# Performance work log

Measured on AMD Instinct MI355X. Metric: run time of the kernel, lower is better.

Reference implementation:

```python
import jax, jax.numpy as jnp
import numpy as np

N = 50000        # nodes
E = 1600000      # edges (before self loops)
IN_DIM = 300     # input feature size
HID = 256        # hidden size
HEADS = 8
OC = HID // HEADS  # out channels per head = 32
LAYERS = 4
B = 1024         # number of target pairs
C = 3            # num classes
NEG_SLOPE = 0.2  # PyG GATConv leaky_relu slope


def setup_inputs() -> dict:
    key = jax.random.key(0)
    ks = jax.random.split(key, 12)

    def glorot(k, shape):
        lim = np.sqrt(6.0 / (shape[-2] + shape[-1]))
        return jax.random.uniform(k, shape, jnp.float32, -lim, lim)

    return {
        "x": jax.random.normal(ks[0], (N, IN_DIM), jnp.float32),
        "edge_index": jax.random.randint(ks[1], (2, E), 0, N, jnp.int64 if jax.config.jax_enable_x64 else jnp.int32),
        "target_mask": jax.random.randint(ks[2], (B, 2), 0, N, jnp.int64 if jax.config.jax_enable_x64 else jnp.int32),
        # lin1: [IN_DIM, HID] (stored pre-transposed vs torch)
        "lin1_W": glorot(ks[3], (IN_DIM, HID)),
        "lin1_b": jnp.zeros((HID,), jnp.float32),
        # stacked GATConv params
        "convs_W": glorot(ks[4], (LAYERS, HID, HEADS * OC)),
        "convs_att_dst": glorot(ks[5], (LAYERS, HEADS, OC)),  # att half applied to x_i (target)
        "convs_att_src": glorot(ks[6], (LAYERS, HEADS, OC)),  # att half applied to x_j (source)
        "convs_b": jnp.zeros((LAYERS, HID), jnp.float32),
        # lin3: [2*HID, C]
        "lin3_W": glorot(ks[7], (2 * HID, C)),
        "lin3_b": jnp.zeros((C,), jnp.float32),
    }


def gat_layer(h, src, tgt, W, att_dst, att_src, bias):
    """PyG-style GATConv (concat heads), edge list already includes self loops.
    h: [N, HID]; src/tgt: [E+N]; W: [HID, HEADS*OC]."""
    hw = (h @ W).reshape(N, HEADS, OC)
    # per-node attention scores, gathered per-edge (avoids materializing concat features)
    s_dst = jnp.einsum("nho,ho->nh", hw, att_dst)  # score for target role
    s_src = jnp.einsum("nho,ho->nh", hw, att_src)  # score for source role
    alpha = jax.nn.leaky_relu(s_dst[tgt] + s_src[src], NEG_SLOPE)  # [Etot, HEADS]
    # softmax over edges sharing the same target node (self loops => no empty segments)
    m = jax.ops.segment_max(alpha, tgt, num_segments=N)
    ex = jnp.exp(alpha - m[tgt])
    denom = jax.ops.segment_sum(ex, tgt, num_segments=N)
    a = ex / (denom[tgt] + 1e-16)
    # weighted scatter-aggregate of source features
    out = jax.ops.segment_sum(hw[src] * a[:, :, None], tgt, num_segments=N)  # [N, HEADS, OC]
    return out.reshape(N, HEADS * OC) + bias


def reference(x, edge_index, target_mask, lin1_W, lin1_b, convs_W,
              convs_att_dst, convs_att_src, convs_b, lin3_W, lin3_b):
    # add self loops once (PyG GATConv does this per layer; same edge set every layer)
    loop = jnp.arange(N, dtype=edge_index.dtype)
    src = jnp.concatenate([edge_index[0], loop])
    tgt = jnp.concatenate([edge_index[1], loop])

    h = x @ lin1_W + lin1_b
    for l in range(LAYERS):
        h = jax.nn.elu(gat_layer(h, src, tgt, convs_W[l],
                                 convs_att_dst[l], convs_att_src[l], convs_b[l]))
    # gather the two target nodes per sample and flatten -> [B, 2*HID]
    feats = h[target_mask].reshape(B, 2 * HID)
    logits = feats @ lin3_W + lin3_b
    return logits
```

## Files before the change

kernel.cpp:

```cpp
#include <hip/hip_runtime.h>
#include <math.h>

#define N_NODES 50000
#define N_PAD   50048
#define E_EDGES 1600000
#define ETOT    (E_EDGES + N_NODES)
#define EPAD    (E_EDGES + 8 * N_NODES)
#define IN_DIM  300
#define KP1     320
#define HID     256
#define HEADS   8
#define OC      32
#define LAYERS  4
#define BSAMP   1024
#define NEG_SLOPE 0.2f
#define DEG_CAP 128

typedef _Float16 half8 __attribute__((ext_vector_type(8)));
typedef _Float16 half4v __attribute__((ext_vector_type(4)));
typedef float f32x4 __attribute__((ext_vector_type(4)));


__global__ __launch_bounds__(256) void init_counts_kernel(int* counts) {
    int i = blockIdx.x * 256 + threadIdx.x;
    if (i < N_NODES) counts[i] = 1;
}

__global__ __launch_bounds__(256) void count_edges_kernel(const int* __restrict__ tgt, int* counts) {
    int e = blockIdx.x * 256 + threadIdx.x;
    if (e < E_EDGES) atomicAdd(&counts[tgt[e]], 1);
}

__global__ __launch_bounds__(256) void scan_kernel(const int* __restrict__ counts,
                                                   int* __restrict__ row_ptr,
                                                   int* __restrict__ cursor) {
    __shared__ int sums[256];
    const int CHUNK = (N_NODES + 255) / 256;
    int t = threadIdx.x;
    int beg = t * CHUNK;
    int fin = min(beg + CHUNK, N_NODES);
    int s = 0;
    for (int i = beg; i < fin; i++) s += (counts[i] + 7) & ~7;
    sums[t] = s;
    __syncthreads();
    for (int off = 1; off < 256; off <<= 1) {
        int a = sums[t];
        int u = (t >= off) ? sums[t - off] : 0;
        __syncthreads();
        sums[t] = a + u;
        __syncthreads();
    }
    int running = sums[t] - s;
    for (int i = beg; i < fin; i++) {
        row_ptr[i] = running;
        cursor[i]  = running;
        running += (counts[i] + 7) & ~7;
    }
    if (t == 255) row_ptr[N_NODES] = sums[255];
}

__global__ __launch_bounds__(256) void fill_edges_kernel(const int* __restrict__ src,
                                                         const int* __restrict__ tgt,
                                                         int* cursor, int* __restrict__ col) {
    int e = blockIdx.x * 256 + threadIdx.x;
    if (e >= ETOT) return;
    int s_, t_;
    if (e < E_EDGES) { s_ = src[e]; t_ = tgt[e]; }
    else             { s_ = t_ = e - E_EDGES; }
    int pos = atomicAdd(&cursor[t_], 1);
    col[pos] = s_;
}

__global__ __launch_bounds__(256) void pad_edges_kernel(const int* __restrict__ cursor,
                                                        const int* __restrict__ row_ptr,
                                                        int* __restrict__ col) {
    int i = blockIdx.x * 256 + threadIdx.x;
    if (i >= N_NODES) return;
    int e = cursor[i];
    int pe = row_ptr[i + 1];
    for (; e < pe; e++) col[e] = i;
}


__global__ __launch_bounds__(256) void cast_x_kernel(const float* __restrict__ x, _Float16* __restrict__ xh) {
    long i = (long)blockIdx.x * 256 + threadIdx.x;
    if (i >= (long)N_NODES * KP1) return;
    int r = (int)(i / KP1), c = (int)(i % KP1);
    float v = (c < IN_DIM) ? x[(size_t)r * IN_DIM + c] : 0.f;
    xh[i] = (_Float16)v;
}

__global__ __launch_bounds__(256) void cast_w1_kernel(const float* __restrict__ W, _Float16* __restrict__ Wt) {
    int i = blockIdx.x * 256 + threadIdx.x;
    if (i >= HID * KP1) return;
    int n = i / KP1, k = i % KP1;
    float v = (k < IN_DIM) ? W[(size_t)k * HID + n] : 0.f;
    Wt[i] = (_Float16)v;
}

__global__ __launch_bounds__(256) void cast_wc_kernel(const float* __restrict__ W, _Float16* __restrict__ Wt) {
    int i = blockIdx.x * 256 + threadIdx.x;
    if (i >= LAYERS * HID * HID) return;
    int l = i / (HID * HID);
    int r = i % (HID * HID);
    int n = r / HID, k = r % HID;
    Wt[i] = (_Float16)W[(size_t)l * HID * HID + (size_t)k * HID + n];
}

__global__ __launch_bounds__(256) void gemm_mfma_kernel(const _Float16* __restrict__ A,
                                                        const _Float16* __restrict__ Wt,
                                                        const float* __restrict__ bias,
                                                        _Float16* __restrict__ C,
                                                        int M, int Kp, int addbias) {
    __shared__ _Float16 As[128][32];
    __shared__ _Float16 Bs[128][32];
    const int tid = threadIdx.x;
    const int m0 = blockIdx.x * 128;
    const int n0 = blockIdx.y * 128;
    const int w = tid >> 6, lane = tid & 63;
    const int wm = (w & 1) * 64, wn = (w >> 1) * 64;
    const int quad = lane >> 4, m16 = lane & 15;

    f32x4 acc[4][4];
    #pragma unroll
    for (int i = 0; i < 4; i++)
        #pragma unroll
        for (int j = 0; j < 4; j++)
            acc[i][j] = (f32x4){0.f, 0.f, 0.f, 0.f};

    for (int k0 = 0; k0 < Kp; k0 += 32) {
        #pragma unroll
        for (int i = 0; i < 2; i++) {
            int seg = tid + i * 256;
            int row = seg >> 2, off = seg & 3;
            uint4 v = *(const uint4*)&A[(size_t)(m0 + row) * Kp + k0 + off * 8];
            *(uint4*)&As[row][off * 8] = v;
            uint4 u = *(const uint4*)&Wt[(size_t)(n0 + row) * Kp + k0 + off * 8];
            *(uint4*)&Bs[row][off * 8] = u;
        }
        __syncthreads();

        half8 af[4], bf[4];
        #pragma unroll
        for (int i = 0; i < 4; i++) {
            af[i] = *(const half8*)&As[wm + i * 16 + m16][quad * 8];
            bf[i] = *(const half8*)&Bs[wn + i * 16 + m16][quad * 8];
        }
        #pragma unroll
        for (int mi = 0; mi < 4; mi++)
            #pragma unroll
            for (int ni = 0; ni < 4; ni++)
                acc[mi][ni] = __builtin_amdgcn_mfma_f32_16x16x32_f16(af[mi], bf[ni], acc[mi][ni], 0, 0, 0);
        __syncthreads();
    }

    #pragma unroll
    for (int mi = 0; mi < 4; mi++) {
        #pragma unroll
        for (int r = 0; r < 4; r++) {
            int row = m0 + wm + mi * 16 + quad * 4 + r;
            if (row < M) {
                #pragma unroll
                for (int ni = 0; ni < 4; ni++) {
                    int colg = n0 + wn + ni * 16 + m16;
                    float v = acc[mi][ni][r];
                    if (addbias) v += bias[colg];
                    C[(size_t)row * HID + colg] = (_Float16)v;
                }
            }
        }
    }
}

__global__ __launch_bounds__(256) void score_kernel(const _Float16* __restrict__ hw,
                                                    const float* __restrict__ att_dst,
                                                    const float* __restrict__ att_src,
                                                    float* __restrict__ s_dst,
                                                    float* __restrict__ s_src) {
    int n = blockIdx.x;
    int c = threadIdx.x;
    float v  = (float)hw[(size_t)n * HID + c];
    float vd = v * att_dst[c];
    float vs = v * att_src[c];
    #pragma unroll
    for (int off = 16; off >= 1; off >>= 1) {
        vd += __shfl_xor(vd, off);
        vs += __shfl_xor(vs, off);
    }
    if ((c & 31) == 0) {
        int h = c >> 5;
        s_dst[(size_t)n * HEADS + h] = vd;
        s_src[(size_t)n * HEADS + h] = vs;
    }
}

__global__ __launch_bounds__(256) void agg_kernel(const int* __restrict__ row_ptr,
                                                  const int* __restrict__ deg_arr,
                                                  const int* __restrict__ col,
                                                  const float* __restrict__ s_dst,
                                                  const float* __restrict__ s_src,
                                                  const _Float16* __restrict__ hw,
                                                  const float* __restrict__ bias,
                                                  _Float16* __restrict__ h_out) {
    __shared__ float aL[4][DEG_CAP * 8];
    __shared__ int  snL[4][DEG_CAP];

    int wv   = threadIdx.x >> 6;
    int lane = threadIdx.x & 63;
    int t = blockIdx.x * 4 + wv;
    if (t >= N_NODES) return;

    int start = row_ptr[t];
    int pdeg  = row_ptr[t + 1] - start;
    int deg   = deg_arr[t];

    int eh  = lane & 7;
    int ech = lane >> 3;
    float sd = s_dst[(size_t)t * HEADS + eh];

    if (pdeg <= DEG_CAP) {
        float mx = -1e30f;
        int ngrp = pdeg >> 3;
        for (int g = 0; g < ngrp; g++) {
            int slot = g * 8 + ech;
            int sn = col[start + slot];
            float a = sd + s_src[(size_t)sn * HEADS + eh];
            a = (a > 0.f) ? a : NEG_SLOPE * a;
            aL[wv][slot * 8 + eh] = a;
            if (eh == 0) snL[wv][slot] = sn;
            if (slot < deg) mx = fmaxf(mx, a);
        }
        mx = fmaxf(mx, __shfl_xor(mx, 8));
        mx = fmaxf(mx, __shfl_xor(mx, 16));
        mx = fmaxf(mx, __shfl_xor(mx, 32));

        int p  = lane >> 5;
        int c  = lane & 31;
        int hh = c >> 2;
        float mxc = __shfl(mx, hh);

        const half8* hw8 = (const half8*)hw;
        float acc[8] = {0.f, 0.f, 0.f, 0.f, 0.f, 0.f, 0.f, 0.f};
        float dsum = 0.f;

        for (int g = 0; g < ngrp; g++) {
            int base = g * 8;
            int   sns[4];
            half8 v[4];
            float ex[4];
            #pragma unroll
            for (int j = 0; j < 4; j++) sns[j] = snL[wv][base + 2 * j + p];
            #pragma unroll
            for (int j = 0; j < 4; j++) v[j] = hw8[(size_t)sns[j] * 32 + c];
            #pragma unroll
            for (int j = 0; j < 4; j++) {
                int slot = base + 2 * j + p;
                float a = aL[wv][slot * 8 + hh];
                ex[j] = (slot < deg) ? __expf(a - mxc) : 0.f;
                dsum += ex[j];
            }
            #pragma unroll
            for (int j = 0; j < 4; j++)
                #pragma unroll
                for (int i = 0; i < 8; i++)
                    acc[i] += ex[j] * (float)v[j][i];
        }

        dsum += __shfl_xor(dsum, 32);
        #pragma unroll
        for (int i = 0; i < 8; i++) acc[i] += __shfl_xor(acc[i], 32);

        float inv = 1.f / (dsum + 1e-16f);
        if (p == 0) {
            half8 ov;
            #pragma unroll
            for (int i = 0; i < 8; i++) {
                float o = acc[i] * inv + bias[c * 8 + i];
                o = (o > 0.f) ? o : (__expf(o) - 1.f);
                ov[i] = (_Float16)o;
            }
            ((half8*)h_out)[(size_t)t * 32 + c] = ov;
        }
    } else {
        int end = start + deg;
        float mx = -1e30f;
        for (int base = start; base < end; base += 8) {
            int e = base + ech;
            if (e < end) {
                int sn = col[e];
                float a = sd + s_src[(size_t)sn * HEADS + eh];
                a = (a > 0.f) ? a : NEG_SLOPE * a;
                mx = fmaxf(mx, a);
            }
        }
        mx = fmaxf(mx, __shfl_xor(mx, 8));
        mx = fmaxf(mx, __shfl_xor(mx, 16));
        mx = fmaxf(mx, __shfl_xor(mx, 32));

        float4 acc = {0.f, 0.f, 0.f, 0.f};
        float dsum = 0.f;
        const half4v* hw4 = (const half4v*)hw;
        int chead = lane >> 3;
        for (int base = start; base < end; base += 8) {
            int e = base + ech;
            float exv = 0.f;
            int sn = 0;
            if (e < end) {
                sn = col[e];
                float a = sd + s_src[(size_t)sn * HEADS + eh];
                a = (a > 0.f) ? a : NEG_SLOPE * a;
                exv = __expf(a - mx);
                dsum += exv;
            }
            int cnt = min(8, end - base);
            for (int j = 0; j < cnt; j++) {
                float exj = __shfl(exv, j * 8 + chead);
                int  snj  = __shfl(sn,  j * 8);
                half4v v = hw4[(size_t)snj * 64 + lane];
                acc.x += exj * (float)v[0];
                acc.y += exj * (float)v[1];
                acc.z += exj * (float)v[2];
                acc.w += exj * (float)v[3];
            }
        }
        dsum += __shfl_xor(dsum, 8);
        dsum += __shfl_xor(dsum, 16);
        dsum += __shfl_xor(dsum, 32);
        float den = __shfl(dsum, chead) + 1e-16f;
        float inv = 1.f / den;
        int cb = lane * 4;
        float o[4] = {acc.x * inv + bias[cb + 0], acc.y * inv + bias[cb + 1],
                      acc.z * inv + bias[cb + 2], acc.w * inv + bias[cb + 3]};
        #pragma unroll
        for (int i = 0; i < 4; i++) o[i] = (o[i] > 0.f) ? o[i] : (__expf(o[i]) - 1.f);
        half4v ov;
        ov[0] = (_Float16)o[0]; ov[1] = (_Float16)o[1];
        ov[2] = (_Float16)o[2]; ov[3] = (_Float16)o[3];
        ((half4v*)h_out)[(size_t)t * 64 + lane] = ov;
    }
}

__global__ __launch_bounds__(256) void head_kernel(const _Float16* __restrict__ h,
                                                   const int* __restrict__ target_mask,
                                                   const float* __restrict__ W,
                                                   const float* __restrict__ b,
                                                   float* __restrict__ out) {
    int s = blockIdx.x;
    int t = threadIdx.x;
    int n0 = target_mask[s * 2 + 0];
    int n1 = target_mask[s * 2 + 1];
    float f0 = (float)h[(size_t)n0 * HID + t];
    float f1 = (float)h[(size_t)n1 * HID + t];
    float a0 = f0 * W[t * 3 + 0] + f1 * W[(t + 256) * 3 + 0];
    float a1 = f0 * W[t * 3 + 1] + f1 * W[(t + 256) * 3 + 1];
    float a2 = f0 * W[t * 3 + 2] + f1 * W[(t + 256) * 3 + 2];
    #pragma unroll
    for (int off = 32; off >= 1; off >>= 1) {
        a0 += __shfl_xor(a0, off);
        a1 += __shfl_xor(a1, off);
        a2 += __shfl_xor(a2, off);
    }
    __shared__ float red[4][3];
    int wv = t >> 6, ln = t & 63;
    if (ln == 0) { red[wv][0] = a0; red[wv][1] = a1; red[wv][2] = a2; }
    __syncthreads();
    if (t < 3) {
        out[s * 3 + t] = red[0][t] + red[1][t] + red[2][t] + red[3][t] + b[t];
    }
}


extern "C" void kernel_launch(void* const* d_in, const int* in_sizes, int n_in,
                              void* d_out, int out_size, void* d_ws, size_t ws_size,
                              hipStream_t stream) {
    const float* x        = (const float*)d_in[0];
    const int*   eidx     = (const int*)  d_in[1];
    const int*   tmask    = (const int*)  d_in[2];
    const float* lin1_W   = (const float*)d_in[3];
    const float* lin1_b   = (const float*)d_in[4];
    const float* convs_W  = (const float*)d_in[5];
    const float* att_dst  = (const float*)d_in[6];
    const float* att_src  = (const float*)d_in[7];
    const float* convs_b  = (const float*)d_in[8];
    const float* lin3_W   = (const float*)d_in[9];
    const float* lin3_b   = (const float*)d_in[10];
    float* out = (float*)d_out;

    char* ws = (char*)d_ws;
    size_t off = 0;
    auto alloc = [&](size_t bytes) -> void* {
        void* p = ws + off;
        off = (off + bytes + 255) & ~(size_t)255;
        return p;
    };
    _Float16* xh   = (_Float16*)alloc((size_t)N_PAD * KP1 * 2);
    _Float16* h    = (_Float16*)alloc((size_t)N_PAD * HID * 2);
    _Float16* hw   = (_Float16*)alloc((size_t)N_NODES * HID * 2);
    _Float16* w1t  = (_Float16*)alloc((size_t)HID * KP1 * 2);
    _Float16* wct  = (_Float16*)alloc((size_t)LAYERS * HID * HID * 2);
    float* sdst    = (float*)alloc((size_t)N_NODES * HEADS * 4);
    float* ssrc    = (float*)alloc((size_t)N_NODES * HEADS * 4);
    int*   counts  = (int*)  alloc((size_t)N_NODES * 4);
    int*   rowptr  = (int*)  alloc((size_t)(N_NODES + 1) * 4);
    int*   cursor  = (int*)  alloc((size_t)N_NODES * 4);
    int*   col     = (int*)  alloc((size_t)EPAD * 4);

    const int* src = eidx;
    const int* tgt = eidx + E_EDGES;

    init_counts_kernel<<<(N_NODES + 255) / 256, 256, 0, stream>>>(counts);
    count_edges_kernel<<<(E_EDGES + 255) / 256, 256, 0, stream>>>(tgt, counts);
    scan_kernel<<<1, 256, 0, stream>>>(counts, rowptr, cursor);
    fill_edges_kernel<<<(ETOT + 255) / 256, 256, 0, stream>>>(src, tgt, cursor, col);
    pad_edges_kernel<<<(N_NODES + 255) / 256, 256, 0, stream>>>(cursor, rowptr, col);

    cast_x_kernel<<<((long)N_NODES * KP1 + 255) / 256, 256, 0, stream>>>(x, xh);
    cast_w1_kernel<<<(HID * KP1 + 255) / 256, 256, 0, stream>>>(lin1_W, w1t);
    cast_wc_kernel<<<(LAYERS * HID * HID + 255) / 256, 256, 0, stream>>>(convs_W, wct);

    gemm_mfma_kernel<<<dim3((N_NODES + 127) / 128, HID / 128), 256, 0, stream>>>(
        xh, w1t, lin1_b, h, N_NODES, KP1, 1);

    for (int l = 0; l < LAYERS; l++) {
        gemm_mfma_kernel<<<dim3((N_NODES + 127) / 128, HID / 128), 256, 0, stream>>>(
            h, wct + (size_t)l * HID * HID, nullptr, hw, N_NODES, HID, 0);
        score_kernel<<<N_NODES, 256, 0, stream>>>(
            hw, att_dst + (size_t)l * HEADS * OC, att_src + (size_t)l * HEADS * OC, sdst, ssrc);
        agg_kernel<<<(N_NODES + 3) / 4, 256, 0, stream>>>(
            rowptr, counts, col, sdst, ssrc, hw, convs_b + (size_t)l * HID, h);
    }

    head_kernel<<<BSAMP, 256, 0, stream>>>(h, tmask, lin3_W, lin3_b, out);
}
```

Measured before the change: 1.173 ms.

## Bucket edges by target range, batch score computation, drop softmax max pass

```diff
diff --git a/kernel.cpp b/kernel.cpp
--- a/kernel.cpp
+++ b/kernel.cpp
@@ -16,19 +16,60 @@
 #define NEG_SLOPE 0.2f
 #define DEG_CAP 128
 
+#define NB    8
+#define NPB   6250
+#define BCAP  262144
+
+typedef unsigned long long ull;
 typedef _Float16 half8 __attribute__((ext_vector_type(8)));
 typedef _Float16 half4v __attribute__((ext_vector_type(4)));
 typedef float f32x4 __attribute__((ext_vector_type(4)));
 
 
-__global__ __launch_bounds__(256) void init_counts_kernel(int* counts) {
-    int i = blockIdx.x * 256 + threadIdx.x;
-    if (i < N_NODES) counts[i] = 1;
-}
-
-__global__ __launch_bounds__(256) void count_edges_kernel(const int* __restrict__ tgt, int* counts) {
-    int e = blockIdx.x * 256 + threadIdx.x;
-    if (e < E_EDGES) atomicAdd(&counts[tgt[e]], 1);
+__global__ __launch_bounds__(256) void part_edges_kernel(const int* __restrict__ src,
+                                                         const int* __restrict__ tgt,
+                                                         ull* __restrict__ bpart,
+                                                         int* __restrict__ bcnt) {
+    int lane = threadIdx.x & 63;
+    long stride = (long)gridDim.x * 256;
+    for (long e0 = (long)blockIdx.x * 256; e0 < ETOT; e0 += stride) {
+        long e = e0 + threadIdx.x;
+        int b = -1;
+        ull pk = 0;
+        if (e < ETOT) {
+            int s_, t_;
+            if (e < E_EDGES) { s_ = src[e]; t_ = tgt[e]; }
+            else             { s_ = t_ = (int)(e - E_EDGES); }
+            b = t_ / NPB;
+            pk = ((ull)(unsigned)t_ << 32) | (unsigned)s_;
+        }
+        #pragma unroll
+        for (int bb = 0; bb < NB; bb++) {
+            ull m = __ballot(b == bb);
+            if (m == 0) continue;
+            int ldr = __builtin_ctzll(m);
+            int cnt = __popcll(m);
+            int base = 0;
+            if (lane == ldr) base = atomicAdd(&bcnt[bb], cnt);
+            base = __shfl(base, ldr);
+            if (b == bb) {
+                int rank = __popcll(m & ((1ull << lane) - 1ull));
+                bpart[(size_t)bb * BCAP + base + rank] = pk;
+            }
+        }
+    }
+}
+
+__global__ __launch_bounds__(256) void count_edges_kernel(const ull* __restrict__ bpart,
+                                                          const int* __restrict__ bcnt,
+                                                          int* counts) {
+    int b = blockIdx.x & (NB - 1);
+    int ib = blockIdx.x >> 3;
+    int nblk = gridDim.x >> 3;
+    int nb = bcnt[b];
+    const ull* bp = bpart + (size_t)b * BCAP;
+    for (int i = ib * 256 + threadIdx.x; i < nb; i += nblk * 256)
+        atomicAdd(&counts[(int)(bp[i] >> 32)], 1);
 }
 
 __global__ __launch_bounds__(256) void scan_kernel(const int* __restrict__ counts,
@@ -59,16 +100,21 @@
     if (t == 255) row_ptr[N_NODES] = sums[255];
 }
 
-__global__ __launch_bounds__(256) void fill_edges_kernel(const int* __restrict__ src,
-                                                         const int* __restrict__ tgt,
+__global__ __launch_bounds__(256) void fill_edges_kernel(const ull* __restrict__ bpart,
+                                                         const int* __restrict__ bcnt,
                                                          int* cursor, int* __restrict__ col) {
-    int e = blockIdx.x * 256 + threadIdx.x;
-    if (e >= ETOT) return;
-    int s_, t_;
-    if (e < E_EDGES) { s_ = src[e]; t_ = tgt[e]; }
-    else             { s_ = t_ = e - E_EDGES; }
-    int pos = atomicAdd(&cursor[t_], 1);
-    col[pos] = s_;
+    int b = blockIdx.x & (NB - 1);
+    int ib = blockIdx.x >> 3;
+    int nblk = gridDim.x >> 3;
+    int nb = bcnt[b];
+    const ull* bp = bpart + (size_t)b * BCAP;
+    for (int i = ib * 256 + threadIdx.x; i < nb; i += nblk * 256) {
+        ull pk = bp[i];
+        int t_ = (int)(pk >> 32);
+        int s_ = (int)pk;
+        int pos = atomicAdd(&cursor[t_], 1);
+        col[pos] = s_;
+    }
 }
 
 __global__ __launch_bounds__(256) void pad_edges_kernel(const int* __restrict__ cursor,
@@ -177,20 +223,31 @@
                                                     const float* __restrict__ att_src,
                                                     float* __restrict__ s_dst,
                                                     float* __restrict__ s_src) {
-    int n = blockIdx.x;
-    int c = threadIdx.x;
-    float v  = (float)hw[(size_t)n * HID + c];
-    float vd = v * att_dst[c];
-    float vs = v * att_src[c];
+    int wv = threadIdx.x >> 6, lane = threadIdx.x & 63;
+    int nd = lane >> 3, hd = lane & 7;
+    float4 ad[8], as4[8];
+    const float4* A4d = (const float4*)att_dst;
+    const float4* A4s = (const float4*)att_src;
     #pragma unroll
-    for (int off = 16; off >= 1; off >>= 1) {
-        vd += __shfl_xor(vd, off);
-        vs += __shfl_xor(vs, off);
-    }
-    if ((c & 31) == 0) {
-        int h = c >> 5;
-        s_dst[(size_t)n * HEADS + h] = vd;
-        s_src[(size_t)n * HEADS + h] = vs;
+    for (int j = 0; j < 8; j++) { ad[j] = A4d[hd * 8 + j]; as4[j] = A4s[hd * 8 + j]; }
+    const half8* hw8 = (const half8*)hw;
+    int nwaves = gridDim.x * 4;
+    for (int g = blockIdx.x * 4 + wv; g < N_NODES / 8; g += nwaves) {
+        int node = g * 8 + nd;
+        float sd = 0.f, ss = 0.f;
+        #pragma unroll
+        for (int k = 0; k < 4; k++) {
+            half8 v = hw8[(size_t)node * 32 + hd * 4 + k];
+            #pragma unroll
+            for (int i = 0; i < 8; i++) {
+                float f = (float)v[i];
+                int q = k * 8 + i;
+                sd += f * ((const float*)&ad[q >> 2])[q & 3];
+                ss += f * ((const float*)&as4[q >> 2])[q & 3];
+            }
+        }
+        s_dst[(size_t)g * 64 + lane] = sd;
+        s_src[(size_t)g * 64 + lane] = ss;
     }
 }
 
@@ -202,7 +259,7 @@
                                                   const _Float16* __restrict__ hw,
                                                   const float* __restrict__ bias,
                                                   _Float16* __restrict__ h_out) {
-    __shared__ float aL[4][DEG_CAP * 8];
+    __shared__ float exL[4][DEG_CAP * 8];
     __shared__ int  snL[4][DEG_CAP];
 
     int wv   = threadIdx.x >> 6;
@@ -219,29 +276,29 @@
     float sd = s_dst[(size_t)t * HEADS + eh];
 
     if (pdeg <= DEG_CAP) {
-        float mx = -1e30f;
         int ngrp = pdeg >> 3;
+        float dsum = 0.f;
         for (int g = 0; g < ngrp; g++) {
             int slot = g * 8 + ech;
             int sn = col[start + slot];
             float a = sd + s_src[(size_t)sn * HEADS + eh];
             a = (a > 0.f) ? a : NEG_SLOPE * a;
-            aL[wv][slot * 8 + eh] = a;
+            float exv = (slot < deg) ? __expf(a) : 0.f;
+            exL[wv][slot * 8 + eh] = exv;
             if (eh == 0) snL[wv][slot] = sn;
-            if (slot < deg) mx = fmaxf(mx, a);
-        }
-        mx = fmaxf(mx, __shfl_xor(mx, 8));
-        mx = fmaxf(mx, __shfl_xor(mx, 16));
-        mx = fmaxf(mx, __shfl_xor(mx, 32));
+            dsum += exv;
+        }
+        dsum += __shfl_xor(dsum, 8);
+        dsum += __shfl_xor(dsum, 16);
+        dsum += __shfl_xor(dsum, 32);
 
         int p  = lane >> 5;
         int c  = lane & 31;
         int hh = c >> 2;
-        float mxc = __shfl(mx, hh);
+        float inv = 1.f / (__shfl(dsum, hh) + 1e-16f);
 
         const half8* hw8 = (const half8*)hw;
         float acc[8] = {0.f, 0.f, 0.f, 0.f, 0.f, 0.f, 0.f, 0.f};
-        float dsum = 0.f;
 
         for (int g = 0; g < ngrp; g++) {
             int base = g * 8;
@@ -253,12 +310,7 @@
             #pragma unroll
             for (int j = 0; j < 4; j++) v[j] = hw8[(size_t)sns[j] * 32 + c];
             #pragma unroll
-            for (int j = 0; j < 4; j++) {
-                int slot = base + 2 * j + p;
-                float a = aL[wv][slot * 8 + hh];
-                ex[j] = (slot < deg) ? __expf(a - mxc) : 0.f;
-                dsum += ex[j];
-            }
+            for (int j = 0; j < 4; j++) ex[j] = exL[wv][(base + 2 * j + p) * 8 + hh];
             #pragma unroll
             for (int j = 0; j < 4; j++)
                 #pragma unroll
@@ -266,11 +318,9 @@
                     acc[i] += ex[j] * (float)v[j][i];
         }
 
-        dsum += __shfl_xor(dsum, 32);
         #pragma unroll
         for (int i = 0; i < 8; i++) acc[i] += __shfl_xor(acc[i], 32);
 
-        float inv = 1.f / (dsum + 1e-16f);
         if (p == 0) {
             half8 ov;
             #pragma unroll
@@ -404,14 +454,18 @@
     int*   rowptr  = (int*)  alloc((size_t)(N_NODES + 1) * 4);
     int*   cursor  = (int*)  alloc((size_t)N_NODES * 4);
     int*   col     = (int*)  alloc((size_t)EPAD * 4);
+    ull*   bpart   = (ull*)  alloc((size_t)NB * BCAP * 8);
+    int*   bcnt    = (int*)  alloc((size_t)NB * 4);
 
     const int* src = eidx;
     const int* tgt = eidx + E_EDGES;
 
-    init_counts_kernel<<<(N_NODES + 255) / 256, 256, 0, stream>>>(counts);
-    count_edges_kernel<<<(E_EDGES + 255) / 256, 256, 0, stream>>>(tgt, counts);
+    hipMemsetAsync(counts, 0, (size_t)N_NODES * 4, stream);
+    hipMemsetAsync(bcnt, 0, (size_t)NB * 4, stream);
+    part_edges_kernel<<<1024, 256, 0, stream>>>(src, tgt, bpart, bcnt);
+    count_edges_kernel<<<256, 256, 0, stream>>>(bpart, bcnt, counts);
     scan_kernel<<<1, 256, 0, stream>>>(counts, rowptr, cursor);
-    fill_edges_kernel<<<(ETOT + 255) / 256, 256, 0, stream>>>(src, tgt, cursor, col);
+    fill_edges_kernel<<<256, 256, 0, stream>>>(bpart, bcnt, cursor, col);
     pad_edges_kernel<<<(N_NODES + 255) / 256, 256, 0, stream>>>(cursor, rowptr, col);
 
     cast_x_kernel<<<((long)N_NODES * KP1 + 255) / 256, 256, 0, stream>>>(x, xh);
@@ -424,7 +478,7 @@
     for (int l = 0; l < LAYERS; l++) {
         gemm_mfma_kernel<<<dim3((N_NODES + 127) / 128, HID / 128), 256, 0, stream>>>(
             h, wct + (size_t)l * HID * HID, nullptr, hw, N_NODES, HID, 0);
-        score_kernel<<<N_NODES, 256, 0, stream>>>(
+        score_kernel<<<256, 256, 0, stream>>>(
             hw, att_dst + (size_t)l * HEADS * OC, att_src + (size_t)l * HEADS * OC, sdst, ssrc);
         agg_kernel<<<(N_NODES + 3) / 4, 256, 0, stream>>>(
             rowptr, counts, col, sdst, ssrc, hw, convs_b + (size_t)l * HID, h);
```

Measured after the change: 3.338 ms. +184.4%, slower.
